# Kernel tuning notes

Measured on AMD Instinct MI355X. Metric: run time of the kernel, lower is better.

The kernel has to match this reference:

```python
import jax, jax.numpy as jnp
import numpy as np

B, T, D, E, TOP_K = 4, 4096, 1024, 8, 2
CAPACITY_FACTOR = 1.5


def setup_inputs() -> dict:
    key = jax.random.key(0)
    k1, k2, k3 = jax.random.split(key, 3)
    x = jax.random.normal(k1, (B, T, D), dtype=jnp.float32)
    Wr = jax.random.normal(k2, (E, D), dtype=jnp.float32) * 0.02   # router weight [E, D]
    We = jax.random.normal(k3, (E, D, D), dtype=jnp.float32) * 0.02  # per-expert dense [E, D, D]
    return {"x": x, "Wr": Wr, "We": We}


def reference(x, Wr, We):
    Bb, Tt, Dd = x.shape
    Ee = Wr.shape[0]
    K = TOP_K
    C = int(Tt * K / Ee * CAPACITY_FACTOR) + 1  # max_tokens_per_expert

    # Router + fused top-k softmax (triton_topk_softmax semantics)
    logits = jnp.einsum('btd,ed->bte', x, Wr)                 # [B, T, E]
    top_vals, top_idx = jax.lax.top_k(logits, K)              # [B, T, K]
    w = jax.nn.softmax(top_vals, axis=-1)                     # [B, T, K]

    # Position of each (token, k) slot inside its expert's capacity buffer,
    # assigned in (t, k) order -- matches the sequential counter in _build_position_map.
    flat_e = top_idx.reshape(Bb, Tt * K)                      # [B, T*K]
    oh = jax.nn.one_hot(flat_e, Ee, dtype=jnp.int32)          # [B, T*K, E]
    pos_all = jnp.cumsum(oh, axis=1) - oh                     # count of earlier slots per expert
    pos = jnp.take_along_axis(pos_all, flat_e[..., None], axis=-1)[..., 0]  # [B, T*K]
    keep = pos < C                                            # capacity drop

    # Scatter tokens into [B, E, C, D] capacity buffers (triton_expert_scatter)
    b_idx = jnp.arange(Bb, dtype=jnp.int32)[:, None]
    dst = (b_idx * Ee + flat_e) * C + pos                     # flat buffer index
    dst = jnp.where(keep, dst, Bb * Ee * C).reshape(-1)       # out-of-range -> dropped
    x_rep = jnp.repeat(x, K, axis=1).reshape(-1, Dd)          # [B*T*K, D]
    buf = jnp.zeros((Bb * Ee * C, Dd), dtype=x.dtype).at[dst].add(x_rep, mode='drop')
    expert_in = buf.reshape(Bb, Ee, C, Dd)

    # expert_fn: per-expert dense layer (grouped GEMM)
    expert_out = jnp.einsum('becd,edf->becf', expert_in, We)  # [B, E, C, D]

    # Gather back + weighted combine (triton_expert_gather)
    gathered = jnp.take(expert_out.reshape(Bb * Ee * C, Dd), dst, axis=0,
                        mode='fill', fill_value=0.0)          # dropped slots -> 0
    gathered = gathered.reshape(Bb, Tt, K, Dd)
    out = jnp.einsum('btk,btkd->btd', w, gathered)            # [B, T, D]
    return out
```

## Files before the change

kernel.cpp:

```cpp
#include <hip/hip_runtime.h>
#include <hip/hip_bf16.h>
#include <math.h>

#define B_ 4
#define T_ 4096
#define D_ 1024
#define E_ 8
#define K_ 2
#define C_ 1537

typedef short bf16x8 __attribute__((ext_vector_type(8)));
typedef float f32x4 __attribute__((ext_vector_type(4)));

__device__ __forceinline__ unsigned short f2bf(float f) {
    union { float f; unsigned int u; } c; c.f = f;
    unsigned int u = c.u;
    unsigned int r = (u + 0x7fffu + ((u >> 16) & 1u)) >> 16;
    return (unsigned short)r;
}

__global__ __launch_bounds__(256) void router_kernel(
    const float* __restrict__ x, const float* __restrict__ Wr,
    unsigned short* __restrict__ xbf, int* __restrict__ top_e,
    float* __restrict__ wbuf) {
    __shared__ float wr_s[E_ * D_];
    int tid = threadIdx.x;
    const float4* wr4 = (const float4*)Wr;
    float4* wrs4 = (float4*)wr_s;
    for (int i = tid; i < E_ * D_ / 4; i += 256) wrs4[i] = wr4[i];
    __syncthreads();

    int wave = tid >> 6, lane = tid & 63;
    int token = blockIdx.x * 4 + wave;

    const float4* xr = (const float4*)(x + (size_t)token * D_) + lane * 4;
    float xs[16];
    #pragma unroll
    for (int i = 0; i < 4; i++) {
        float4 v = xr[i];
        xs[i * 4 + 0] = v.x; xs[i * 4 + 1] = v.y;
        xs[i * 4 + 2] = v.z; xs[i * 4 + 3] = v.w;
    }

    unsigned short xb[16];
    #pragma unroll
    for (int i = 0; i < 16; i++) xb[i] = f2bf(xs[i]);
    uint4* dst = (uint4*)(xbf + (size_t)token * D_ + lane * 16);
    dst[0] = ((uint4*)xb)[0];
    dst[1] = ((uint4*)xb)[1];

    double acc[E_];
    #pragma unroll
    for (int e = 0; e < E_; e++) {
        const float* wp = wr_s + e * D_ + lane * 16;
        double a = 0.0;
        #pragma unroll
        for (int i = 0; i < 16; i++) a += (double)xs[i] * (double)wp[i];
        acc[e] = a;
    }
    #pragma unroll
    for (int e = 0; e < E_; e++) {
        #pragma unroll
        for (int off = 32; off > 0; off >>= 1)
            acc[e] += __shfl_down(acc[e], off, 64);
    }

    if (lane == 0) {
        int e0 = 0; double v0 = acc[0];
        #pragma unroll
        for (int e = 1; e < E_; e++) if (acc[e] > v0) { v0 = acc[e]; e0 = e; }
        int e1 = -1; double v1 = -1.0e300;
        #pragma unroll
        for (int e = 0; e < E_; e++) if (e != e0 && acc[e] > v1) { v1 = acc[e]; e1 = e; }
        double ex = exp(v1 - v0);
        float w0 = (float)(1.0 / (1.0 + ex));
        float w1 = (float)(ex / (1.0 + ex));
        top_e[token * 2 + 0] = e0;
        top_e[token * 2 + 1] = e1;
        wbuf[token * 2 + 0] = w0;
        wbuf[token * 2 + 1] = w1;
    }
}

__global__ __launch_bounds__(256) void wt_kernel(const float* __restrict__ We,
                                                 unsigned short* __restrict__ wtbf) {
    __shared__ unsigned short tile[64][65];
    int e = blockIdx.x >> 8;
    int t = blockIdx.x & 255;
    int d0 = (t >> 4) * 64, f0 = (t & 15) * 64;
    const float* src = We + ((size_t)e * D_ + d0) * D_ + f0;
    int tid = threadIdx.x;
    #pragma unroll
    for (int i = 0; i < 16; i++) {
        int idx = tid + i * 256;
        int r = idx >> 6, c = idx & 63;
        tile[r][c] = f2bf(src[(size_t)r * D_ + c]);
    }
    __syncthreads();
    unsigned short* dstp = wtbf + ((size_t)e * D_ + f0) * D_ + d0;
    #pragma unroll
    for (int i = 0; i < 16; i++) {
        int idx = tid + i * 256;
        int r = idx >> 6, c = idx & 63;
        dstp[(size_t)r * D_ + c] = tile[c][r];
    }
}

__global__ __launch_bounds__(256) void scan_kernel(const int* __restrict__ top_e,
                                                   int* __restrict__ list,
                                                   int* __restrict__ count) {
    int b = blockIdx.x, tid = threadIdx.x;
    const int S = T_ * K_;
    const int per = S / 256;
    __shared__ int cnt[256][E_];
    int local[E_];
    #pragma unroll
    for (int e = 0; e < E_; e++) local[e] = 0;
    const int* te = top_e + (size_t)b * S + tid * per;
    int evals[32];
    for (int i = 0; i < per; i++) { evals[i] = te[i]; local[evals[i]]++; }
    #pragma unroll
    for (int e = 0; e < E_; e++) cnt[tid][e] = local[e];
    __syncthreads();
    if (tid < E_) {
        int run = 0;
        for (int i = 0; i < 256; i++) { int v = cnt[i][tid]; cnt[i][tid] = run; run += v; }
        count[b * E_ + tid] = min(run, C_);
    }
    __syncthreads();
    int base[E_];
    #pragma unroll
    for (int e = 0; e < E_; e++) base[e] = cnt[tid][e];
    int* lst = list + (size_t)b * E_ * C_;
    for (int i = 0; i < per; i++) {
        int ev = evals[i];
        int p = base[ev]++;
        if (p < C_) lst[ev * C_ + p] = tid * per + i;
    }
}

#define LDA 40

__global__ __launch_bounds__(256) void gemm_kernel(
    const unsigned short* __restrict__ xbf, const unsigned short* __restrict__ wtbf,
    const int* __restrict__ list, const int* __restrict__ count,
    const float* __restrict__ wbuf, float* __restrict__ out) {
    int cb = blockIdx.x & 7;
    int rb = (blockIdx.x >> 3) % 13;
    int pe = blockIdx.x / 104;
    int b = pe >> 3, e = pe & 7;
    int cnt = count[pe];
    int row0 = rb * 128;
    if (row0 >= cnt) return;
    int rows = min(128, cnt - row0);

    __shared__ unsigned short As[128 * LDA];
    __shared__ unsigned short Bs[128 * LDA];
    __shared__ int slots[128];

    int tid = threadIdx.x;
    if (tid < 128) slots[tid] = (tid < rows) ? list[pe * C_ + row0 + tid] : 0;
    __syncthreads();

    int chunk = tid & 3;
    int r0 = tid >> 2;
    int r1 = r0 + 64;
    int tA0 = slots[r0] >> 1, tA1 = slots[r1] >> 1;
    const uint4* a0 = (const uint4*)(xbf + ((size_t)b * T_ + tA0) * D_) + chunk;
    const uint4* a1 = (const uint4*)(xbf + ((size_t)b * T_ + tA1) * D_) + chunk;
    const uint4* b0 = (const uint4*)(wtbf + ((size_t)e * D_ + cb * 128 + r0) * D_) + chunk;
    const uint4* b1 = (const uint4*)(wtbf + ((size_t)e * D_ + cb * 128 + r1) * D_) + chunk;
    uint4* sa0 = (uint4*)(As + r0 * LDA + chunk * 8);
    uint4* sa1 = (uint4*)(As + r1 * LDA + chunk * 8);
    uint4* sb0 = (uint4*)(Bs + r0 * LDA + chunk * 8);
    uint4* sb1 = (uint4*)(Bs + r1 * LDA + chunk * 8);

    int wave = tid >> 6, lane = tid & 63;
    int wm = wave >> 1, wn = wave & 1;
    int quad = lane >> 4, mrow = lane & 15;
    const unsigned short* ArdBase = As + (wm * 64 + mrow) * LDA + quad * 8;
    const unsigned short* BrdBase = Bs + (wn * 64 + mrow) * LDA + quad * 8;

    f32x4 acc[4][4];
    #pragma unroll
    for (int i = 0; i < 4; i++)
        #pragma unroll
        for (int j = 0; j < 4; j++) acc[i][j] = (f32x4){0.f, 0.f, 0.f, 0.f};

    uint4 ra0 = a0[0], ra1 = a1[0], rb0 = b0[0], rb1 = b1[0];

    for (int kk = 0; kk < 32; kk++) {
        __syncthreads();
        *sa0 = ra0; *sa1 = ra1; *sb0 = rb0; *sb1 = rb1;
        if (kk < 31) {
            ra0 = a0[(kk + 1) * 4];
            ra1 = a1[(kk + 1) * 4];
            rb0 = b0[(kk + 1) * 4];
            rb1 = b1[(kk + 1) * 4];
        }
        __syncthreads();
        bf16x8 af[4], bfv[4];
        #pragma unroll
        for (int i = 0; i < 4; i++)
            af[i] = *(const bf16x8*)(ArdBase + i * 16 * LDA);
        #pragma unroll
        for (int j = 0; j < 4; j++)
            bfv[j] = *(const bf16x8*)(BrdBase + j * 16 * LDA);
        #pragma unroll
        for (int i = 0; i < 4; i++)
            #pragma unroll
            for (int j = 0; j < 4; j++)
                acc[i][j] = __builtin_amdgcn_mfma_f32_16x16x32_bf16(af[i], bfv[j], acc[i][j], 0, 0, 0);
    }

    float* outb = out + (size_t)b * T_ * D_;
    const float* wb = wbuf + (size_t)b * T_ * 2;
    int ncolbase = cb * 128 + wn * 64 + mrow;
    #pragma unroll
    for (int i = 0; i < 4; i++) {
        #pragma unroll
        for (int r = 0; r < 4; r++) {
            int m = wm * 64 + i * 16 + quad * 4 + r;
            if (m < rows) {
                int s = slots[m];
                int t = s >> 1;
                float wgt = wb[t * 2 + (s & 1)];
                float* orow = outb + (size_t)t * D_;
                #pragma unroll
                for (int j = 0; j < 4; j++)
                    atomicAdd(orow + ncolbase + j * 16, wgt * acc[i][j][r]);
            }
        }
    }
}

extern "C" void kernel_launch(void* const* d_in, const int* in_sizes, int n_in,
                              void* d_out, int out_size, void* d_ws, size_t ws_size,
                              hipStream_t stream) {
    const float* x  = (const float*)d_in[0];
    const float* Wr = (const float*)d_in[1];
    const float* We = (const float*)d_in[2];
    float* out = (float*)d_out;
    char* ws = (char*)d_ws;

    unsigned short* xbf  = (unsigned short*)(ws);
    unsigned short* wtbf = (unsigned short*)(ws + 33554432);
    int*   top_e = (int*)  (ws + 50331648);
    float* wbuf  = (float*)(ws + 50462720);
    int*   list  = (int*)  (ws + 50593792);
    int*   count = (int*)  (ws + 50790528);

    hipMemsetAsync(d_out, 0, (size_t)out_size * sizeof(float), stream);
    router_kernel<<<dim3(B_ * T_ / 4), dim3(256), 0, stream>>>(x, Wr, xbf, top_e, wbuf);
    wt_kernel<<<dim3(E_ * 256), dim3(256), 0, stream>>>(We, wtbf);
    scan_kernel<<<dim3(B_), dim3(256), 0, stream>>>(top_e, list, count);
    gemm_kernel<<<dim3(32 * 13 * 8), dim3(256), 0, stream>>>(xbf, wtbf, list, count, wbuf, out);
}
```

Before: 328.3 us.

## Replace atomic scatter-combine with bf16 gather buffer and separate combine kernel

The GEMM now writes un-weighted bf16 expert outputs into a per-slot buffer instead of atomically adding weighted fp32 results into the output. A new combine kernel applies the routing weights and a keep mask, which removes the output memset and the atomics. The GEMM itself moves to 256-row tiles with direct global-to-LDS loads of the gathered A rows, double buffering, and B fragments held in registers. The router handles four tokens per wave with a butterfly reduction, and the scan uses a wave-level prefix sum. The cost is an extra 64 MB bf16 round trip through the gather buffer and bf16 rounding of expert outputs before weighting.

```diff
diff --git a/kernel.cpp b/kernel.cpp
--- a/kernel.cpp
+++ b/kernel.cpp
@@ -15,8 +15,15 @@
 __device__ __forceinline__ unsigned short f2bf(float f) {
     union { float f; unsigned int u; } c; c.f = f;
     unsigned int u = c.u;
-    unsigned int r = (u + 0x7fffu + ((u >> 16) & 1u)) >> 16;
-    return (unsigned short)r;
+    return (unsigned short)((u + 0x7fffu + ((u >> 16) & 1u)) >> 16);
+}
+__device__ __forceinline__ float bf2f(unsigned short u) {
+    union { unsigned int i; float f; } c; c.i = ((unsigned int)u) << 16;
+    return c.f;
+}
+__device__ __forceinline__ void ldsdma16(const void* g, void* l) {
+    __builtin_amdgcn_global_load_lds((const __attribute__((address_space(1))) void*)g,
+                                     (__attribute__((address_space(3))) void*)l, 16, 0, 0);
 }
 
 __global__ __launch_bounds__(256) void router_kernel(
@@ -27,58 +34,79 @@
     int tid = threadIdx.x;
     const float4* wr4 = (const float4*)Wr;
     float4* wrs4 = (float4*)wr_s;
-    for (int i = tid; i < E_ * D_ / 4; i += 256) wrs4[i] = wr4[i];
+    #pragma unroll
+    for (int i = 0; i < 8; i++) wrs4[tid + i * 256] = wr4[tid + i * 256];
     __syncthreads();
 
     int wave = tid >> 6, lane = tid & 63;
-    int token = blockIdx.x * 4 + wave;
-
-    const float4* xr = (const float4*)(x + (size_t)token * D_) + lane * 4;
-    float xs[16];
-    #pragma unroll
-    for (int i = 0; i < 4; i++) {
-        float4 v = xr[i];
-        xs[i * 4 + 0] = v.x; xs[i * 4 + 1] = v.y;
-        xs[i * 4 + 2] = v.z; xs[i * 4 + 3] = v.w;
-    }
-
-    unsigned short xb[16];
-    #pragma unroll
-    for (int i = 0; i < 16; i++) xb[i] = f2bf(xs[i]);
-    uint4* dst = (uint4*)(xbf + (size_t)token * D_ + lane * 16);
-    dst[0] = ((uint4*)xb)[0];
-    dst[1] = ((uint4*)xb)[1];
-
-    double acc[E_];
-    #pragma unroll
-    for (int e = 0; e < E_; e++) {
-        const float* wp = wr_s + e * D_ + lane * 16;
-        double a = 0.0;
-        #pragma unroll
-        for (int i = 0; i < 16; i++) a += (double)xs[i] * (double)wp[i];
-        acc[e] = a;
-    }
-    #pragma unroll
-    for (int e = 0; e < E_; e++) {
-        #pragma unroll
-        for (int off = 32; off > 0; off >>= 1)
-            acc[e] += __shfl_down(acc[e], off, 64);
-    }
-
-    if (lane == 0) {
-        int e0 = 0; double v0 = acc[0];
-        #pragma unroll
-        for (int e = 1; e < E_; e++) if (acc[e] > v0) { v0 = acc[e]; e0 = e; }
-        int e1 = -1; double v1 = -1.0e300;
-        #pragma unroll
-        for (int e = 0; e < E_; e++) if (e != e0 && acc[e] > v1) { v1 = acc[e]; e1 = e; }
-        double ex = exp(v1 - v0);
-        float w0 = (float)(1.0 / (1.0 + ex));
-        float w1 = (float)(ex / (1.0 + ex));
-        top_e[token * 2 + 0] = e0;
-        top_e[token * 2 + 1] = e1;
-        wbuf[token * 2 + 0] = w0;
-        wbuf[token * 2 + 1] = w1;
+    int h5 = (lane >> 5) & 1, h4 = (lane >> 4) & 1, h3 = (lane >> 3) & 1;
+
+    for (int tt = 0; tt < 4; tt++) {
+        int token = blockIdx.x * 16 + wave * 4 + tt;
+        const float4* xr = (const float4*)(x + (size_t)token * D_) + lane * 4;
+        float xs[16];
+        #pragma unroll
+        for (int i = 0; i < 4; i++) {
+            float4 v = xr[i];
+            xs[i * 4 + 0] = v.x; xs[i * 4 + 1] = v.y;
+            xs[i * 4 + 2] = v.z; xs[i * 4 + 3] = v.w;
+        }
+        unsigned short xb[16];
+        #pragma unroll
+        for (int i = 0; i < 16; i++) xb[i] = f2bf(xs[i]);
+        uint4* dst = (uint4*)(xbf + (size_t)token * D_ + lane * 16);
+        dst[0] = ((uint4*)xb)[0];
+        dst[1] = ((uint4*)xb)[1];
+
+        double acc[E_];
+        #pragma unroll
+        for (int e = 0; e < E_; e++) {
+            const float* wp = wr_s + e * D_ + lane * 16;
+            double a = 0.0;
+            #pragma unroll
+            for (int i = 0; i < 16; i++) a += (double)xs[i] * (double)wp[i];
+            acc[e] = a;
+        }
+        double r4[4];
+        #pragma unroll
+        for (int i = 0; i < 4; i++) {
+            double send = h5 ? acc[i] : acc[4 + i];
+            double keep = h5 ? acc[4 + i] : acc[i];
+            r4[i] = keep + __shfl_xor(send, 32, 64);
+        }
+        double r2[2];
+        #pragma unroll
+        for (int i = 0; i < 2; i++) {
+            double send = h4 ? r4[i] : r4[2 + i];
+            double keep = h4 ? r4[2 + i] : r4[i];
+            r2[i] = keep + __shfl_xor(send, 16, 64);
+        }
+        double r1;
+        {
+            double send = h3 ? r2[0] : r2[1];
+            double keep = h3 ? r2[1] : r2[0];
+            r1 = keep + __shfl_xor(send, 8, 64);
+        }
+        r1 += __shfl_xor(r1, 4, 64);
+        r1 += __shfl_xor(r1, 2, 64);
+        r1 += __shfl_xor(r1, 1, 64);
+        double le[E_];
+        #pragma unroll
+        for (int e = 0; e < E_; e++) le[e] = __shfl(r1, e << 3, 64);
+
+        if (lane == 0) {
+            int e0 = 0; double v0 = le[0];
+            #pragma unroll
+            for (int e = 1; e < E_; e++) if (le[e] > v0) { v0 = le[e]; e0 = e; }
+            int e1 = -1; double v1 = -1.0e300;
+            #pragma unroll
+            for (int e = 0; e < E_; e++) if (e != e0 && le[e] > v1) { v1 = le[e]; e1 = e; }
+            double ex = exp(v1 - v0);
+            top_e[token * 2 + 0] = e0;
+            top_e[token * 2 + 1] = e1;
+            wbuf[token * 2 + 0] = (float)(1.0 / (1.0 + ex));
+            wbuf[token * 2 + 1] = (float)(ex / (1.0 + ex));
+        }
     }
 }
 
@@ -108,130 +136,178 @@
 
 __global__ __launch_bounds__(256) void scan_kernel(const int* __restrict__ top_e,
                                                    int* __restrict__ list,
-                                                   int* __restrict__ count) {
+                                                   int* __restrict__ count,
+                                                   unsigned char* __restrict__ keep8) {
     int b = blockIdx.x, tid = threadIdx.x;
-    const int S = T_ * K_;
-    const int per = S / 256;
-    __shared__ int cnt[256][E_];
+    const int per = 32;
+    __shared__ int cnt[256][9];
     int local[E_];
     #pragma unroll
     for (int e = 0; e < E_; e++) local[e] = 0;
-    const int* te = top_e + (size_t)b * S + tid * per;
+    const int* te = top_e + (size_t)b * 8192 + tid * per;
     int evals[32];
     for (int i = 0; i < per; i++) { evals[i] = te[i]; local[evals[i]]++; }
     #pragma unroll
     for (int e = 0; e < E_; e++) cnt[tid][e] = local[e];
     __syncthreads();
-    if (tid < E_) {
-        int run = 0;
-        for (int i = 0; i < 256; i++) { int v = cnt[i][tid]; cnt[i][tid] = run; run += v; }
-        count[b * E_ + tid] = min(run, C_);
-    }
-    __syncthreads();
+
+    int wave = tid >> 6, lane = tid & 63;
+    #pragma unroll
+    for (int ee = 0; ee < 2; ee++) {
+        int e = wave * 2 + ee;
+        int s0 = cnt[lane * 4 + 0][e], s1 = cnt[lane * 4 + 1][e];
+        int s2 = cnt[lane * 4 + 2][e], s3 = cnt[lane * 4 + 3][e];
+        int tot = s0 + s1 + s2 + s3;
+        int s = tot;
+        #pragma unroll
+        for (int off = 1; off < 64; off <<= 1) {
+            int t2 = __shfl_up(s, off, 64);
+            if (lane >= off) s += t2;
+        }
+        int base = s - tot;
+        cnt[lane * 4 + 0][e] = base;
+        cnt[lane * 4 + 1][e] = base + s0;
+        cnt[lane * 4 + 2][e] = base + s0 + s1;
+        cnt[lane * 4 + 3][e] = base + s0 + s1 + s2;
+        if (lane == 63) count[b * E_ + e] = min(s, C_);
+    }
+    __syncthreads();
+
     int base[E_];
     #pragma unroll
     for (int e = 0; e < E_; e++) base[e] = cnt[tid][e];
     int* lst = list + (size_t)b * E_ * C_;
+    unsigned char* kp = keep8 + (size_t)b * 8192;
     for (int i = 0; i < per; i++) {
         int ev = evals[i];
         int p = base[ev]++;
-        if (p < C_) lst[ev * C_ + p] = tid * per + i;
-    }
-}
-
-#define LDA 40
-
-__global__ __launch_bounds__(256) void gemm_kernel(
+        int slot = tid * per + i;
+        kp[slot] = (p < C_) ? 1 : 0;
+        if (p < C_) lst[ev * C_ + p] = slot;
+    }
+}
+
+__global__ __launch_bounds__(256, 2) void gemm_kernel(
     const unsigned short* __restrict__ xbf, const unsigned short* __restrict__ wtbf,
     const int* __restrict__ list, const int* __restrict__ count,
-    const float* __restrict__ wbuf, float* __restrict__ out) {
-    int cb = blockIdx.x & 7;
-    int rb = (blockIdx.x >> 3) % 13;
-    int pe = blockIdx.x / 104;
+    unsigned short* __restrict__ gbuf) {
+    int cb = blockIdx.x;
+    int rb = blockIdx.y;
+    int pe = blockIdx.z;
     int b = pe >> 3, e = pe & 7;
     int cnt = count[pe];
-    int row0 = rb * 128;
+    int row0 = rb * 256;
     if (row0 >= cnt) return;
-    int rows = min(128, cnt - row0);
-
-    __shared__ unsigned short As[128 * LDA];
-    __shared__ unsigned short Bs[128 * LDA];
-    __shared__ int slots[128];
+    int rows = min(256, cnt - row0);
+
+    __shared__ unsigned short Abuf[2][256 * 32];
+    __shared__ unsigned int rowByte[256];
+    __shared__ int slotArr[256];
 
     int tid = threadIdx.x;
-    if (tid < 128) slots[tid] = (tid < rows) ? list[pe * C_ + row0 + tid] : 0;
-    __syncthreads();
-
-    int chunk = tid & 3;
-    int r0 = tid >> 2;
-    int r1 = r0 + 64;
-    int tA0 = slots[r0] >> 1, tA1 = slots[r1] >> 1;
-    const uint4* a0 = (const uint4*)(xbf + ((size_t)b * T_ + tA0) * D_) + chunk;
-    const uint4* a1 = (const uint4*)(xbf + ((size_t)b * T_ + tA1) * D_) + chunk;
-    const uint4* b0 = (const uint4*)(wtbf + ((size_t)e * D_ + cb * 128 + r0) * D_) + chunk;
-    const uint4* b1 = (const uint4*)(wtbf + ((size_t)e * D_ + cb * 128 + r1) * D_) + chunk;
-    uint4* sa0 = (uint4*)(As + r0 * LDA + chunk * 8);
-    uint4* sa1 = (uint4*)(As + r1 * LDA + chunk * 8);
-    uint4* sb0 = (uint4*)(Bs + r0 * LDA + chunk * 8);
-    uint4* sb1 = (uint4*)(Bs + r1 * LDA + chunk * 8);
+    {
+        int slot = list[pe * C_ + row0 + min(tid, rows - 1)];
+        slotArr[tid] = (tid < rows) ? slot : -1;
+        rowByte[tid] = (unsigned)(((b << 12) + (slot >> 1)) << 11);
+    }
+    __syncthreads();
 
     int wave = tid >> 6, lane = tid & 63;
     int wm = wave >> 1, wn = wave & 1;
     int quad = lane >> 4, mrow = lane & 15;
-    const unsigned short* ArdBase = As + (wm * 64 + mrow) * LDA + quad * 8;
-    const unsigned short* BrdBase = Bs + (wn * 64 + mrow) * LDA + quad * 8;
-
-    f32x4 acc[4][4];
-    #pragma unroll
-    for (int i = 0; i < 4; i++)
+
+    const char* xbase = (const char*)xbf;
+    unsigned aOff[4];
+    #pragma unroll
+    for (int g = 0; g < 4; g++) {
+        int rg = wave * 4 + g;
+        aOff[g] = rowByte[rg * 16 + mrow] + quad * 16;
+    }
+    const char* wtbase = (const char*)wtbf;
+    unsigned bOff[4];
+    #pragma unroll
+    for (int jt = 0; jt < 4; jt++) {
+        int n = cb * 128 + wn * 64 + jt * 16 + mrow;
+        bOff[jt] = (unsigned)((((e << 10) + n) << 11) + quad * 16);
+    }
+
+    f32x4 acc[8][4];
+    #pragma unroll
+    for (int i = 0; i < 8; i++)
         #pragma unroll
         for (int j = 0; j < 4; j++) acc[i][j] = (f32x4){0.f, 0.f, 0.f, 0.f};
 
-    uint4 ra0 = a0[0], ra1 = a1[0], rb0 = b0[0], rb1 = b1[0];
+    #pragma unroll
+    for (int g = 0; g < 4; g++)
+        ldsdma16(xbase + aOff[g], &Abuf[0][(wave * 4 + g) * 512]);
+    uint4 bcur[4], bnext[4];
+    #pragma unroll
+    for (int jt = 0; jt < 4; jt++) bcur[jt] = *(const uint4*)(wtbase + bOff[jt]);
+    __syncthreads();
 
     for (int kk = 0; kk < 32; kk++) {
+        int nb = (kk + 1) & 1;
+        if (kk < 31) {
+            unsigned ko = (unsigned)(kk + 1) * 64u;
+            #pragma unroll
+            for (int g = 0; g < 4; g++)
+                ldsdma16(xbase + aOff[g] + ko, &Abuf[nb][(wave * 4 + g) * 512]);
+            #pragma unroll
+            for (int jt = 0; jt < 4; jt++)
+                bnext[jt] = *(const uint4*)(wtbase + bOff[jt] + ko);
+        }
+        const unsigned short* ab = Abuf[kk & 1] + wm * 8 * 512 + lane * 8;
+        bf16x8 A8[8];
+        #pragma unroll
+        for (int it = 0; it < 8; it++)
+            A8[it] = *(const bf16x8*)(ab + it * 512);
+        #pragma unroll
+        for (int it = 0; it < 8; it++)
+            #pragma unroll
+            for (int jt = 0; jt < 4; jt++)
+                acc[it][jt] = __builtin_amdgcn_mfma_f32_16x16x32_bf16(
+                    A8[it], *(const bf16x8*)&bcur[jt], acc[it][jt], 0, 0, 0);
+        #pragma unroll
+        for (int jt = 0; jt < 4; jt++) bcur[jt] = bnext[jt];
         __syncthreads();
-        *sa0 = ra0; *sa1 = ra1; *sb0 = rb0; *sb1 = rb1;
-        if (kk < 31) {
-            ra0 = a0[(kk + 1) * 4];
-            ra1 = a1[(kk + 1) * 4];
-            rb0 = b0[(kk + 1) * 4];
-            rb1 = b1[(kk + 1) * 4];
-        }
-        __syncthreads();
-        bf16x8 af[4], bfv[4];
-        #pragma unroll
-        for (int i = 0; i < 4; i++)
-            af[i] = *(const bf16x8*)(ArdBase + i * 16 * LDA);
-        #pragma unroll
-        for (int j = 0; j < 4; j++)
-            bfv[j] = *(const bf16x8*)(BrdBase + j * 16 * LDA);
-        #pragma unroll
-        for (int i = 0; i < 4; i++)
-            #pragma unroll
-            for (int j = 0; j < 4; j++)
-                acc[i][j] = __builtin_amdgcn_mfma_f32_16x16x32_bf16(af[i], bfv[j], acc[i][j], 0, 0, 0);
-    }
-
-    float* outb = out + (size_t)b * T_ * D_;
-    const float* wb = wbuf + (size_t)b * T_ * 2;
-    int ncolbase = cb * 128 + wn * 64 + mrow;
-    #pragma unroll
-    for (int i = 0; i < 4; i++) {
+    }
+
+    int colbase = cb * 128 + wn * 64 + mrow;
+    #pragma unroll
+    for (int it = 0; it < 8; it++) {
+        int mbase = wm * 128 + it * 16 + quad * 4;
         #pragma unroll
         for (int r = 0; r < 4; r++) {
-            int m = wm * 64 + i * 16 + quad * 4 + r;
-            if (m < rows) {
-                int s = slots[m];
-                int t = s >> 1;
-                float wgt = wb[t * 2 + (s & 1)];
-                float* orow = outb + (size_t)t * D_;
+            int m = mbase + r;
+            int slot = slotArr[m];
+            if (slot >= 0) {
+                unsigned short* grow = gbuf + ((size_t)((b << 13) + slot) << 10);
                 #pragma unroll
-                for (int j = 0; j < 4; j++)
-                    atomicAdd(orow + ncolbase + j * 16, wgt * acc[i][j][r]);
+                for (int jt = 0; jt < 4; jt++)
+                    grow[colbase + jt * 16] = f2bf(acc[it][jt][r]);
             }
         }
     }
+}
+
+__global__ __launch_bounds__(256) void combine_kernel(
+    const unsigned short* __restrict__ gbuf, const float* __restrict__ wbuf,
+    const unsigned char* __restrict__ keep8, float* __restrict__ out) {
+    int t = blockIdx.x;
+    int b = t >> 12;
+    int tid = threadIdx.x;
+    int kb = (b << 13) + ((t & 4095) << 1);
+    float w0 = wbuf[t * 2 + 0] * (float)keep8[kb + 0];
+    float w1 = wbuf[t * 2 + 1] * (float)keep8[kb + 1];
+    const ushort4* g0 = (const ushort4*)(gbuf + ((size_t)kb << 10)) + tid;
+    const ushort4* g1 = (const ushort4*)(gbuf + (((size_t)kb + 1) << 10)) + tid;
+    ushort4 a = *g0, c = *g1;
+    float4 o;
+    o.x = w0 * bf2f(a.x) + w1 * bf2f(c.x);
+    o.y = w0 * bf2f(a.y) + w1 * bf2f(c.y);
+    o.z = w0 * bf2f(a.z) + w1 * bf2f(c.z);
+    o.w = w0 * bf2f(a.w) + w1 * bf2f(c.w);
+    ((float4*)(out + (size_t)t * D_))[tid] = o;
 }
 
 extern "C" void kernel_launch(void* const* d_in, const int* in_sizes, int n_in,
@@ -245,14 +321,16 @@
 
     unsigned short* xbf  = (unsigned short*)(ws);
     unsigned short* wtbf = (unsigned short*)(ws + 33554432);
-    int*   top_e = (int*)  (ws + 50331648);
-    float* wbuf  = (float*)(ws + 50462720);
-    int*   list  = (int*)  (ws + 50593792);
-    int*   count = (int*)  (ws + 50790528);
-
-    hipMemsetAsync(d_out, 0, (size_t)out_size * sizeof(float), stream);
-    router_kernel<<<dim3(B_ * T_ / 4), dim3(256), 0, stream>>>(x, Wr, xbf, top_e, wbuf);
+    unsigned short* gbuf = (unsigned short*)(ws + 50331648);
+    int*   top_e = (int*)  (ws + 117440512);
+    float* wbuf  = (float*)(ws + 117571584);
+    int*   list  = (int*)  (ws + 117702656);
+    int*   count = (int*)  (ws + 117899392);
+    unsigned char* keep8 = (unsigned char*)(ws + 117899520);
+
+    router_kernel<<<dim3(B_ * T_ / 16), dim3(256), 0, stream>>>(x, Wr, xbf, top_e, wbuf);
     wt_kernel<<<dim3(E_ * 256), dim3(256), 0, stream>>>(We, wtbf);
-    scan_kernel<<<dim3(B_), dim3(256), 0, stream>>>(top_e, list, count);
-    gemm_kernel<<<dim3(32 * 13 * 8), dim3(256), 0, stream>>>(xbf, wtbf, list, count, wbuf, out);
-}
+    scan_kernel<<<dim3(B_), dim3(256), 0, stream>>>(top_e, list, count, keep8);
+    gemm_kernel<<<dim3(8, 7, 32), dim3(256), 0, stream>>>(xbf, wtbf, list, count, gbuf);
+    combine_kernel<<<dim3(B_ * T_), dim3(256), 0, stream>>>(gbuf, wbuf, keep8, out);
+}
```

Result: slower. 394.1 us (+20.0%).
